# Performance work log

Hardware: AMD Instinct MI355X
Metric: run time of the kernel (lower is better)

Reference implementation:

```python
import jax, jax.numpy as jnp
import numpy as np

D = 256          # d_embed
KD = 256         # key_d_embed
NHEAD = 8
DK = D // NHEAD  # 32
QH = QW = 128
QWS = 16
KH = KW = 64
KWS = 8
R = QWS // KWS   # qk_ratio = 2
SCALE = 1.0 / np.sqrt(DK)


def _rel_index():
    # query coords on fine grid, key coords scaled up by ratio R
    qc = np.stack(np.meshgrid(np.arange(QWS), np.arange(QWS), indexing='ij'), -1).reshape(-1, 2)
    kc = np.stack(np.meshgrid(np.arange(KWS), np.arange(KWS), indexing='ij'), -1).reshape(-1, 2) * R
    rel = qc[:, None, :] - kc[None, :, :] + (QWS - R)  # values in [0, 2*QWS-R-1]
    return jnp.asarray(rel[..., 0] * (2 * QWS - R) + rel[..., 1])  # (QWS^2, KWS^2)


def _partition(t, ws):
    # (B, h, H, W, d) -> (B, h, H/ws, W/ws, ws*ws, d)
    B, h, H, W, d = t.shape
    t = t.reshape(B, h, H // ws, ws, W // ws, ws, d).transpose(0, 1, 2, 4, 3, 5, 6)
    return t.reshape(B, h, H // ws, W // ws, ws * ws, d)


def _merge(t, ws, H, W):
    # inverse of _partition
    B, h, nH, nW, _, d = t.shape
    t = t.reshape(B, h, nH, nW, ws, ws, d).transpose(0, 1, 2, 4, 3, 5, 6)
    return t.reshape(B, h, H, W, d)


def setup_inputs() -> dict:
    key = jax.random.key(0)
    ks = jax.random.split(key, 9)
    x = jax.random.normal(ks[0], (8, QH, QW, D), dtype=jnp.float32)
    z = jax.random.normal(ks[1], (8, KH, KW, KD), dtype=jnp.float32)
    mask = jax.random.randint(ks[2], (1, NHEAD, QH // QWS, QW // QWS, QWS * QWS, KWS * KWS), 0, 2) == 1
    Wq = jax.random.normal(ks[3], (D, D), dtype=jnp.float32) * 0.02
    bq = jnp.zeros((D,), dtype=jnp.float32)
    Wkv = jax.random.normal(ks[4], (KD, 2 * D), dtype=jnp.float32) * 0.02
    bkv = jnp.zeros((2 * D,), dtype=jnp.float32)
    Wo = jax.random.normal(ks[5], (D, D), dtype=jnp.float32) * 0.02
    bo = jnp.zeros((D,), dtype=jnp.float32)
    rel_table = jax.random.normal(ks[6], ((2 * QWS - R) ** 2, NHEAD), dtype=jnp.float32) * 0.02
    return {"x": x, "z": z, "mask": mask, "Wq": Wq, "bq": bq, "Wkv": Wkv, "bkv": bkv, "Wo": Wo, "bo": bo, "rel_table": rel_table}


def reference(x, z, mask, Wq, bq, Wkv, bkv, Wo, bo, rel_table):
    B, H, W, _ = x.shape
    q = (x @ Wq + bq).reshape(B, H, W, NHEAD, DK).transpose(0, 3, 1, 2, 4)        # (B,h,H,W,dk)
    kv = (z @ Wkv + bkv).reshape(B, KH, KW, 2, NHEAD, DK).transpose(3, 0, 4, 1, 2, 5)
    k, v = kv[0], kv[1]                                                           # (B,h,_H,_W,dk)
    sq, sk = QWS // 2, KWS // 2
    q = jnp.roll(q, (-sq, -sq), axis=(2, 3))
    k = jnp.roll(k, (-sk, -sk), axis=(2, 3))
    v = jnp.roll(v, (-sk, -sk), axis=(2, 3))
    q = _partition(q, QWS)   # (B,h,nh,nw,QWS^2,dk)
    k = _partition(k, KWS)   # (B,h,nh,nw,KWS^2,dk)
    v = _partition(v, KWS)
    attn = jnp.einsum('bhnmqd,bhnmkd->bhnmqk', q, k) * SCALE
    bias = rel_table[_rel_index()].transpose(2, 0, 1)[None, :, None, None]        # (1,h,1,1,QWS^2,KWS^2)
    attn = attn + bias
    attn = jnp.where(mask, jnp.float32(-1e9), attn)
    attn = jax.nn.softmax(attn, axis=-1)
    out = jnp.einsum('bhnmqk,bhnmkd->bhnmqd', attn, v)
    out = _merge(out, QWS, H, W)
    out = jnp.roll(out, (sq, sq), axis=(2, 3))
    out = out.transpose(0, 2, 3, 1, 4).reshape(B, H, W, D)
    return out @ Wo + bo
```

## Files before the change

kernel.cpp:

```cpp
#include <hip/hip_runtime.h>
#include <hip/hip_bf16.h>
#include <type_traits>


typedef __attribute__((ext_vector_type(8))) short short8v;
typedef __attribute__((ext_vector_type(4))) float f32x4;
typedef __attribute__((ext_vector_type(8))) unsigned short ushort8v;
typedef __attribute__((ext_vector_type(4))) unsigned short ushort4v;

#define DEV __device__ __forceinline__

DEV unsigned short f2bf(float f) {
    union { float f; unsigned u; } v; v.f = f;
    unsigned r = v.u + 0x7FFFu + ((v.u >> 16) & 1u);
    return (unsigned short)(r >> 16);
}

__global__ void prep_weights(const float* __restrict__ Wq, const float* __restrict__ Wkv,
                             const float* __restrict__ Wo,
                             unsigned short* __restrict__ WqT, unsigned short* __restrict__ WkvT,
                             unsigned short* __restrict__ WoT) {
    int idx = blockIdx.x * 256 + threadIdx.x;
    if (idx < 65536) {
        int n = idx >> 8, k = idx & 255;
        WqT[idx] = f2bf(Wq[k * 256 + n]);
    } else if (idx < 196608) {
        int i = idx - 65536;
        int n = i >> 8, k = i & 255;
        WkvT[i] = f2bf(Wkv[k * 512 + n]);
    } else {
        int i = idx - 196608;
        int n = i >> 8, k = i & 255;
        WoT[i] = f2bf(Wo[k * 256 + n]);
    }
}

__global__ void prep_bias(const float* __restrict__ rel_table, float* __restrict__ biasb) {
    int idx = blockIdx.x * 256 + threadIdx.x;
    int head = idx >> 14;
    int q = (idx >> 6) & 255;
    int k = idx & 63;
    int qi = q >> 4, qj = q & 15;
    int ki = k >> 3, kj = k & 7;
    int r0 = qi - 2 * ki + 14, r1 = qj - 2 * kj + 14;
    biasb[idx] = rel_table[(r0 * 30 + r1) * 8 + head];
}

template <typename InT, bool OUT_BF16>
__global__ __launch_bounds__(256) void gemm_proj(
    const InT* __restrict__ A, const unsigned short* __restrict__ BT,
    const float* __restrict__ bias, void* __restrict__ Cout,
    int M, int N, int K)
{
    __shared__ __align__(16) unsigned short As[128][40];
    __shared__ __align__(16) unsigned short Bs[128][40];

    const int tid = threadIdx.x;
    const int mb = blockIdx.y * 128;
    const int nb = blockIdx.x * 128;
    const int w = tid >> 6, lane = tid & 63, lr = lane & 15, lg = lane >> 4;
    const int wm = (w >> 1) * 64, wn = (w & 1) * 64;

    f32x4 acc[4][4];
#pragma unroll
    for (int i = 0; i < 4; ++i)
#pragma unroll
        for (int j = 0; j < 4; ++j) acc[i][j] = {0.f, 0.f, 0.f, 0.f};

    for (int kb = 0; kb < K; kb += 32) {
        if constexpr (std::is_same<InT, float>::value) {
#pragma unroll
            for (int i = 0; i < 4; ++i) {
                int row = (tid >> 3) + i * 32;
                int c4 = (tid & 7) * 4;
                const float4 v = *reinterpret_cast<const float4*>(
                    &A[(size_t)(mb + row) * K + kb + c4]);
                ushort4v u = { f2bf(v.x), f2bf(v.y), f2bf(v.z), f2bf(v.w) };
                *reinterpret_cast<ushort4v*>(&As[row][c4]) = u;
            }
        } else {
#pragma unroll
            for (int i = 0; i < 2; ++i) {
                int flat = tid + i * 256;
                int row = flat >> 2, c8 = (flat & 3) * 8;
                ushort8v v = *reinterpret_cast<const ushort8v*>(
                    &A[(size_t)(mb + row) * K + kb + c8]);
                *reinterpret_cast<ushort8v*>(&As[row][c8]) = v;
            }
        }
#pragma unroll
        for (int i = 0; i < 2; ++i) {
            int flat = tid + i * 256;
            int row = flat >> 2, c8 = (flat & 3) * 8;
            ushort8v v = *reinterpret_cast<const ushort8v*>(
                &BT[(size_t)(nb + row) * K + kb + c8]);
            *reinterpret_cast<ushort8v*>(&Bs[row][c8]) = v;
        }
        __syncthreads();

        short8v af[4], bfr[4];
#pragma unroll
        for (int mt = 0; mt < 4; ++mt)
            af[mt] = *reinterpret_cast<const short8v*>(&As[wm + mt * 16 + lr][lg * 8]);
#pragma unroll
        for (int nt = 0; nt < 4; ++nt)
            bfr[nt] = *reinterpret_cast<const short8v*>(&Bs[wn + nt * 16 + lr][lg * 8]);
#pragma unroll
        for (int mt = 0; mt < 4; ++mt)
#pragma unroll
            for (int nt = 0; nt < 4; ++nt)
                acc[mt][nt] = __builtin_amdgcn_mfma_f32_16x16x32_bf16(
                    af[mt], bfr[nt], acc[mt][nt], 0, 0, 0);
        __syncthreads();
    }

#pragma unroll
    for (int mt = 0; mt < 4; ++mt)
#pragma unroll
        for (int nt = 0; nt < 4; ++nt)
#pragma unroll
            for (int j = 0; j < 4; ++j) {
                int row = mb + wm + mt * 16 + lg * 4 + j;
                int col = nb + wn + nt * 16 + lr;
                float v = acc[mt][nt][j] + bias[col];
                if constexpr (OUT_BF16)
                    ((unsigned short*)Cout)[(size_t)row * N + col] = f2bf(v);
                else
                    ((float*)Cout)[(size_t)row * N + col] = v;
            }
}

__global__ __launch_bounds__(256) void win_attn(
    unsigned short* __restrict__ Qbuf,
    const unsigned short* __restrict__ KVbuf,
    const int* __restrict__ mask,
    const float* __restrict__ biasb)
{
    __shared__ __align__(16) unsigned char sQP[256 * 144];
    __shared__ __align__(16) unsigned short Ks[64][40];
    __shared__ __align__(16) unsigned short Vt[32][72];
    auto Qs = reinterpret_cast<unsigned short(*)[40]>(sQP);
    auto Ps = reinterpret_cast<unsigned short(*)[72]>(sQP);

    const int tid = threadIdx.x;
    const int win = blockIdx.x, head = blockIdx.y, b = blockIdx.z;
    const int wi = win >> 3, wj = win & 7;

    {
        int li = tid >> 4, lj = tid & 15;
        int gr = (wi * 16 + li + 8) & 127;
        int gc = (wj * 16 + lj + 8) & 127;
        const unsigned short* src =
            Qbuf + ((size_t)(b * 16384 + gr * 128 + gc)) * 256 + head * 32;
#pragma unroll
        for (int c = 0; c < 4; ++c)
            *reinterpret_cast<ushort8v*>(&Qs[tid][c * 8]) =
                *reinterpret_cast<const ushort8v*>(src + c * 8);
    }
    if (tid < 64) {
        int ki = tid >> 3, kj = tid & 7;
        int kr = (wi * 8 + ki + 4) & 63;
        int kc = (wj * 8 + kj + 4) & 63;
        const unsigned short* src =
            KVbuf + ((size_t)(b * 4096 + kr * 64 + kc)) * 512 + head * 32;
#pragma unroll
        for (int c = 0; c < 4; ++c)
            *reinterpret_cast<ushort8v*>(&Ks[tid][c * 8]) =
                *reinterpret_cast<const ushort8v*>(src + c * 8);
    } else if (tid < 128) {
        int key = tid - 64;
        int ki = key >> 3, kj = key & 7;
        int kr = (wi * 8 + ki + 4) & 63;
        int kc = (wj * 8 + kj + 4) & 63;
        const unsigned short* src =
            KVbuf + ((size_t)(b * 4096 + kr * 64 + kc)) * 512 + 256 + head * 32;
#pragma unroll
        for (int c = 0; c < 4; ++c) {
            ushort8v v = *reinterpret_cast<const ushort8v*>(src + c * 8);
#pragma unroll
            for (int e = 0; e < 8; ++e) Vt[c * 8 + e][key] = v[e];
        }
    }
    __syncthreads();

    const int w = tid >> 6, lane = tid & 63, lr = lane & 15, lg = lane >> 4;
    const int qb = w * 64;

    short8v qf[4], kf[4];
#pragma unroll
    for (int mt = 0; mt < 4; ++mt)
        qf[mt] = *reinterpret_cast<const short8v*>(&Qs[qb + mt * 16 + lr][lg * 8]);
#pragma unroll
    for (int nt = 0; nt < 4; ++nt)
        kf[nt] = *reinterpret_cast<const short8v*>(&Ks[nt * 16 + lr][lg * 8]);

    f32x4 s[4][4];
#pragma unroll
    for (int mt = 0; mt < 4; ++mt)
#pragma unroll
        for (int nt = 0; nt < 4; ++nt) s[mt][nt] = {0.f, 0.f, 0.f, 0.f};
#pragma unroll
    for (int mt = 0; mt < 4; ++mt)
#pragma unroll
        for (int nt = 0; nt < 4; ++nt)
            s[mt][nt] = __builtin_amdgcn_mfma_f32_16x16x32_bf16(qf[mt], kf[nt], s[mt][nt], 0, 0, 0);

    __syncthreads();

    const float scale = 0.17677669529663687f;
#pragma unroll
    for (int mt = 0; mt < 4; ++mt) {
#pragma unroll
        for (int j = 0; j < 4; ++j) {
            int q = qb + mt * 16 + lg * 4 + j;
            float v[4];
            float m = -3.0e38f;
#pragma unroll
            for (int nt = 0; nt < 4; ++nt) {
                int key = nt * 16 + lr;
                float bi = biasb[(head * 256 + q) * 64 + key];
                int mk = mask[(((head * 64 + win) * 256 + q) * 64) + key];
                float sv = s[mt][nt][j] * scale + bi;
                if (mk) sv = -1.0e9f;
                v[nt] = sv;
                m = fmaxf(m, sv);
            }
#pragma unroll
            for (int d = 1; d < 16; d <<= 1) m = fmaxf(m, __shfl_xor(m, d, 64));
            float sum = 0.f;
#pragma unroll
            for (int nt = 0; nt < 4; ++nt) { v[nt] = __expf(v[nt] - m); sum += v[nt]; }
#pragma unroll
            for (int d = 1; d < 16; d <<= 1) sum += __shfl_xor(sum, d, 64);
            float inv = 1.0f / sum;
#pragma unroll
            for (int nt = 0; nt < 4; ++nt)
                Ps[q][nt * 16 + lr] = f2bf(v[nt] * inv);
        }
    }

    f32x4 o[4][2];
#pragma unroll
    for (int mt = 0; mt < 4; ++mt)
#pragma unroll
        for (int nt = 0; nt < 2; ++nt) o[mt][nt] = {0.f, 0.f, 0.f, 0.f};
#pragma unroll
    for (int kc = 0; kc < 2; ++kc) {
        short8v pf[4], vf[2];
#pragma unroll
        for (int mt = 0; mt < 4; ++mt)
            pf[mt] = *reinterpret_cast<const short8v*>(&Ps[qb + mt * 16 + lr][kc * 32 + lg * 8]);
#pragma unroll
        for (int nt = 0; nt < 2; ++nt)
            vf[nt] = *reinterpret_cast<const short8v*>(&Vt[nt * 16 + lr][kc * 32 + lg * 8]);
#pragma unroll
        for (int mt = 0; mt < 4; ++mt)
#pragma unroll
            for (int nt = 0; nt < 2; ++nt)
                o[mt][nt] = __builtin_amdgcn_mfma_f32_16x16x32_bf16(pf[mt], vf[nt], o[mt][nt], 0, 0, 0);
    }

#pragma unroll
    for (int mt = 0; mt < 4; ++mt)
#pragma unroll
        for (int nt = 0; nt < 2; ++nt)
#pragma unroll
            for (int j = 0; j < 4; ++j) {
                int q = qb + mt * 16 + lg * 4 + j;
                int li = q >> 4, lj = q & 15;
                int gr = (wi * 16 + li + 8) & 127;
                int gc = (wj * 16 + lj + 8) & 127;
                int dk = nt * 16 + lr;
                Qbuf[((size_t)(b * 16384 + gr * 128 + gc)) * 256 + head * 32 + dk] =
                    f2bf(o[mt][nt][j]);
            }
}

extern "C" void kernel_launch(void* const* d_in, const int* in_sizes, int n_in,
                              void* d_out, int out_size, void* d_ws, size_t ws_size,
                              hipStream_t stream) {
    const float* x    = (const float*)d_in[0];
    const float* z    = (const float*)d_in[1];
    const int*   mask = (const int*)d_in[2];
    const float* Wq   = (const float*)d_in[3];
    const float* bq   = (const float*)d_in[4];
    const float* Wkv  = (const float*)d_in[5];
    const float* bkv  = (const float*)d_in[6];
    const float* Wo   = (const float*)d_in[7];
    const float* bo   = (const float*)d_in[8];
    const float* rel  = (const float*)d_in[9];
    float* out = (float*)d_out;

    char* ws = (char*)d_ws;
    unsigned short* Qbuf  = (unsigned short*)(ws);
    unsigned short* KVbuf = (unsigned short*)(ws + 67108864);
    unsigned short* WqT   = (unsigned short*)(ws + 100663296);
    unsigned short* WkvT  = (unsigned short*)(ws + 100794368);
    unsigned short* WoT   = (unsigned short*)(ws + 101056512);
    float*          biasb = (float*)(ws + 101187584);

    prep_weights<<<1024, 256, 0, stream>>>(Wq, Wkv, Wo, WqT, WkvT, WoT);
    prep_bias<<<512, 256, 0, stream>>>(rel, biasb);

    gemm_proj<float, true><<<dim3(2, 1024), 256, 0, stream>>>(
        x, WqT, bq, (void*)Qbuf, 131072, 256, 256);
    gemm_proj<float, true><<<dim3(4, 256), 256, 0, stream>>>(
        z, WkvT, bkv, (void*)KVbuf, 32768, 512, 256);
    win_attn<<<dim3(64, 8, 8), 256, 0, stream>>>(Qbuf, KVbuf, mask, biasb);
    gemm_proj<unsigned short, false><<<dim3(2, 1024), 256, 0, stream>>>(
        Qbuf, WoT, bo, (void*)out, 131072, 256, 256);
}
```

Before: 226.2 us.

## Bit-pack mask, fold scale into Wq, load Q/K fragments directly from global

Packs the int32 attention mask into 64-bit bitmasks once per call, so each row costs one 8-byte load instead of 64 int loads. Folds the softmax scale into Wq and bq during weight prep, and loads the Q and K MFMA fragments straight from global memory instead of staging them in LDS, which removes one barrier. The P buffer gets an XOR swizzle to avoid bank conflicts, and s_setprio is raised around the MFMA blocks. The cost is an extra mask-packing kernel per call and uncoalesced direct global fragment loads.

```diff
diff --git a/kernel.cpp b/kernel.cpp
--- a/kernel.cpp
+++ b/kernel.cpp
@@ -15,6 +15,8 @@
     unsigned r = v.u + 0x7FFFu + ((v.u >> 16) & 1u);
     return (unsigned short)(r >> 16);
 }
+
+#define ATT_SCALE 0.17677669529663687f
 
 __global__ void prep_weights(const float* __restrict__ Wq, const float* __restrict__ Wkv,
                              const float* __restrict__ Wo,
@@ -23,7 +25,7 @@
     int idx = blockIdx.x * 256 + threadIdx.x;
     if (idx < 65536) {
         int n = idx >> 8, k = idx & 255;
-        WqT[idx] = f2bf(Wq[k * 256 + n]);
+        WqT[idx] = f2bf(Wq[k * 256 + n] * ATT_SCALE);
     } else if (idx < 196608) {
         int i = idx - 65536;
         int n = i >> 8, k = i & 255;
@@ -35,15 +37,36 @@
     }
 }
 
-__global__ void prep_bias(const float* __restrict__ rel_table, float* __restrict__ biasb) {
+__global__ void prep_bias(const float* __restrict__ rel_table, const float* __restrict__ bq,
+                          float* __restrict__ biasb, float* __restrict__ bqs) {
     int idx = blockIdx.x * 256 + threadIdx.x;
-    int head = idx >> 14;
-    int q = (idx >> 6) & 255;
-    int k = idx & 63;
-    int qi = q >> 4, qj = q & 15;
-    int ki = k >> 3, kj = k & 7;
-    int r0 = qi - 2 * ki + 14, r1 = qj - 2 * kj + 14;
-    biasb[idx] = rel_table[(r0 * 30 + r1) * 8 + head];
+    if (idx < 131072) {
+        int head = idx >> 14;
+        int q = (idx >> 6) & 255;
+        int k = idx & 63;
+        int qi = q >> 4, qj = q & 15;
+        int ki = k >> 3, kj = k & 7;
+        int r0 = qi - 2 * ki + 14, r1 = qj - 2 * kj + 14;
+        biasb[idx] = rel_table[(r0 * 30 + r1) * 8 + head];
+    } else if (idx < 131328) {
+        int i = idx - 131072;
+        bqs[i] = bq[i] * ATT_SCALE;
+    }
+}
+
+__global__ void prep_mask(const int* __restrict__ mask, unsigned long long* __restrict__ mp) {
+    int idx = blockIdx.x * 256 + threadIdx.x;
+    const int4* src = reinterpret_cast<const int4*>(mask + (size_t)idx * 64);
+    unsigned long long bits = 0;
+#pragma unroll
+    for (int c = 0; c < 16; ++c) {
+        int4 v = src[c];
+        if (v.x) bits |= 1ull << (c * 4 + 0);
+        if (v.y) bits |= 1ull << (c * 4 + 1);
+        if (v.z) bits |= 1ull << (c * 4 + 2);
+        if (v.w) bits |= 1ull << (c * 4 + 3);
+    }
+    mp[idx] = bits;
 }
 
 template <typename InT, bool OUT_BF16>
@@ -133,95 +156,74 @@
 __global__ __launch_bounds__(256) void win_attn(
     unsigned short* __restrict__ Qbuf,
     const unsigned short* __restrict__ KVbuf,
-    const int* __restrict__ mask,
+    const unsigned long long* __restrict__ maskp,
     const float* __restrict__ biasb)
 {
-    __shared__ __align__(16) unsigned char sQP[256 * 144];
-    __shared__ __align__(16) unsigned short Ks[64][40];
+    __shared__ __align__(16) unsigned char Pb[256 * 128];
     __shared__ __align__(16) unsigned short Vt[32][72];
-    auto Qs = reinterpret_cast<unsigned short(*)[40]>(sQP);
-    auto Ps = reinterpret_cast<unsigned short(*)[72]>(sQP);
 
     const int tid = threadIdx.x;
     const int win = blockIdx.x, head = blockIdx.y, b = blockIdx.z;
     const int wi = win >> 3, wj = win & 7;
-
-    {
-        int li = tid >> 4, lj = tid & 15;
-        int gr = (wi * 16 + li + 8) & 127;
-        int gc = (wj * 16 + lj + 8) & 127;
-        const unsigned short* src =
-            Qbuf + ((size_t)(b * 16384 + gr * 128 + gc)) * 256 + head * 32;
-#pragma unroll
-        for (int c = 0; c < 4; ++c)
-            *reinterpret_cast<ushort8v*>(&Qs[tid][c * 8]) =
-                *reinterpret_cast<const ushort8v*>(src + c * 8);
-    }
-    if (tid < 64) {
-        int ki = tid >> 3, kj = tid & 7;
-        int kr = (wi * 8 + ki + 4) & 63;
-        int kc = (wj * 8 + kj + 4) & 63;
-        const unsigned short* src =
-            KVbuf + ((size_t)(b * 4096 + kr * 64 + kc)) * 512 + head * 32;
-#pragma unroll
-        for (int c = 0; c < 4; ++c)
-            *reinterpret_cast<ushort8v*>(&Ks[tid][c * 8]) =
-                *reinterpret_cast<const ushort8v*>(src + c * 8);
-    } else if (tid < 128) {
-        int key = tid - 64;
-        int ki = key >> 3, kj = key & 7;
-        int kr = (wi * 8 + ki + 4) & 63;
-        int kc = (wj * 8 + kj + 4) & 63;
-        const unsigned short* src =
-            KVbuf + ((size_t)(b * 4096 + kr * 64 + kc)) * 512 + 256 + head * 32;
-#pragma unroll
-        for (int c = 0; c < 4; ++c) {
-            ushort8v v = *reinterpret_cast<const ushort8v*>(src + c * 8);
-#pragma unroll
-            for (int e = 0; e < 8; ++e) Vt[c * 8 + e][key] = v[e];
-        }
-    }
-    __syncthreads();
-
     const int w = tid >> 6, lane = tid & 63, lr = lane & 15, lg = lane >> 4;
     const int qb = w * 64;
 
+    {
+        int key = tid & 63, c = tid >> 6;
+        int kr = (wi * 8 + (key >> 3) + 4) & 63;
+        int kc = (wj * 8 + (key & 7) + 4) & 63;
+        ushort8v v = *reinterpret_cast<const ushort8v*>(
+            KVbuf + ((size_t)(b * 4096 + kr * 64 + kc)) * 512 + 256 + head * 32 + c * 8);
+#pragma unroll
+        for (int e = 0; e < 8; ++e) Vt[c * 8 + e][key] = v[e];
+    }
+
     short8v qf[4], kf[4];
 #pragma unroll
-    for (int mt = 0; mt < 4; ++mt)
-        qf[mt] = *reinterpret_cast<const short8v*>(&Qs[qb + mt * 16 + lr][lg * 8]);
-#pragma unroll
-    for (int nt = 0; nt < 4; ++nt)
-        kf[nt] = *reinterpret_cast<const short8v*>(&Ks[nt * 16 + lr][lg * 8]);
+    for (int mt = 0; mt < 4; ++mt) {
+        int q = qb + mt * 16 + lr;
+        int gr = (wi * 16 + (q >> 4) + 8) & 127;
+        int gc = (wj * 16 + (q & 15) + 8) & 127;
+        qf[mt] = *reinterpret_cast<const short8v*>(
+            Qbuf + ((size_t)(b * 16384 + gr * 128 + gc)) * 256 + head * 32 + lg * 8);
+    }
+#pragma unroll
+    for (int nt = 0; nt < 4; ++nt) {
+        int key = nt * 16 + lr;
+        int kr = (wi * 8 + (key >> 3) + 4) & 63;
+        int kc = (wj * 8 + (key & 7) + 4) & 63;
+        kf[nt] = *reinterpret_cast<const short8v*>(
+            KVbuf + ((size_t)(b * 4096 + kr * 64 + kc)) * 512 + head * 32 + lg * 8);
+    }
 
     f32x4 s[4][4];
 #pragma unroll
     for (int mt = 0; mt < 4; ++mt)
 #pragma unroll
         for (int nt = 0; nt < 4; ++nt) s[mt][nt] = {0.f, 0.f, 0.f, 0.f};
+    __builtin_amdgcn_s_setprio(1);
 #pragma unroll
     for (int mt = 0; mt < 4; ++mt)
 #pragma unroll
         for (int nt = 0; nt < 4; ++nt)
             s[mt][nt] = __builtin_amdgcn_mfma_f32_16x16x32_bf16(qf[mt], kf[nt], s[mt][nt], 0, 0, 0);
-
-    __syncthreads();
-
-    const float scale = 0.17677669529663687f;
+    __builtin_amdgcn_s_setprio(0);
+
+    const unsigned long long* mrow = maskp + (size_t)(head * 64 + win) * 256;
 #pragma unroll
     for (int mt = 0; mt < 4; ++mt) {
 #pragma unroll
         for (int j = 0; j < 4; ++j) {
             int q = qb + mt * 16 + lg * 4 + j;
+            unsigned long long mb = mrow[q];
+            const float* brow = biasb + (size_t)(head * 256 + q) * 64;
             float v[4];
             float m = -3.0e38f;
 #pragma unroll
             for (int nt = 0; nt < 4; ++nt) {
                 int key = nt * 16 + lr;
-                float bi = biasb[(head * 256 + q) * 64 + key];
-                int mk = mask[(((head * 64 + win) * 256 + q) * 64) + key];
-                float sv = s[mt][nt][j] * scale + bi;
-                if (mk) sv = -1.0e9f;
+                float sv = s[mt][nt][j] + brow[key];
+                if ((mb >> key) & 1ull) sv = -1.0e9f;
                 v[nt] = sv;
                 m = fmaxf(m, sv);
             }
@@ -233,11 +235,16 @@
 #pragma unroll
             for (int d = 1; d < 16; d <<= 1) sum += __shfl_xor(sum, d, 64);
             float inv = 1.0f / sum;
-#pragma unroll
-            for (int nt = 0; nt < 4; ++nt)
-                Ps[q][nt * 16 + lr] = f2bf(v[nt] * inv);
-        }
-    }
+            int sw = (q & 7) << 4;
+#pragma unroll
+            for (int nt = 0; nt < 4; ++nt) {
+                int off = q * 128 + (((nt * 16 + lr) * 2) ^ sw);
+                *reinterpret_cast<unsigned short*>(Pb + off) = f2bf(v[nt] * inv);
+            }
+        }
+    }
+
+    __syncthreads();
 
     f32x4 o[4][2];
 #pragma unroll
@@ -248,32 +255,36 @@
     for (int kc = 0; kc < 2; ++kc) {
         short8v pf[4], vf[2];
 #pragma unroll
-        for (int mt = 0; mt < 4; ++mt)
-            pf[mt] = *reinterpret_cast<const short8v*>(&Ps[qb + mt * 16 + lr][kc * 32 + lg * 8]);
+        for (int mt = 0; mt < 4; ++mt) {
+            int row = qb + mt * 16 + lr;
+            int coff = (kc * 64 + lg * 16) ^ ((row & 7) << 4);
+            pf[mt] = *reinterpret_cast<const short8v*>(Pb + row * 128 + coff);
+        }
 #pragma unroll
         for (int nt = 0; nt < 2; ++nt)
             vf[nt] = *reinterpret_cast<const short8v*>(&Vt[nt * 16 + lr][kc * 32 + lg * 8]);
+        __builtin_amdgcn_s_setprio(1);
 #pragma unroll
         for (int mt = 0; mt < 4; ++mt)
 #pragma unroll
             for (int nt = 0; nt < 2; ++nt)
                 o[mt][nt] = __builtin_amdgcn_mfma_f32_16x16x32_bf16(pf[mt], vf[nt], o[mt][nt], 0, 0, 0);
-    }
-
-#pragma unroll
-    for (int mt = 0; mt < 4; ++mt)
-#pragma unroll
-        for (int nt = 0; nt < 2; ++nt)
-#pragma unroll
-            for (int j = 0; j < 4; ++j) {
-                int q = qb + mt * 16 + lg * 4 + j;
-                int li = q >> 4, lj = q & 15;
-                int gr = (wi * 16 + li + 8) & 127;
-                int gc = (wj * 16 + lj + 8) & 127;
-                int dk = nt * 16 + lr;
-                Qbuf[((size_t)(b * 16384 + gr * 128 + gc)) * 256 + head * 32 + dk] =
-                    f2bf(o[mt][nt][j]);
-            }
+        __builtin_amdgcn_s_setprio(0);
+    }
+
+#pragma unroll
+    for (int mt = 0; mt < 4; ++mt)
+#pragma unroll
+        for (int j = 0; j < 4; ++j) {
+            int q = qb + mt * 16 + lg * 4 + j;
+            int gr = (wi * 16 + (q >> 4) + 8) & 127;
+            int gc = (wj * 16 + (q & 15) + 8) & 127;
+            unsigned short* dst =
+                Qbuf + ((size_t)(b * 16384 + gr * 128 + gc)) * 256 + head * 32;
+#pragma unroll
+            for (int nt = 0; nt < 2; ++nt)
+                dst[nt * 16 + lr] = f2bf(o[mt][nt][j]);
+        }
 }
 
 extern "C" void kernel_launch(void* const* d_in, const int* in_sizes, int n_in,
@@ -292,21 +303,24 @@
     float* out = (float*)d_out;
 
     char* ws = (char*)d_ws;
-    unsigned short* Qbuf  = (unsigned short*)(ws);
-    unsigned short* KVbuf = (unsigned short*)(ws + 67108864);
-    unsigned short* WqT   = (unsigned short*)(ws + 100663296);
-    unsigned short* WkvT  = (unsigned short*)(ws + 100794368);
-    unsigned short* WoT   = (unsigned short*)(ws + 101056512);
-    float*          biasb = (float*)(ws + 101187584);
+    unsigned short*     Qbuf  = (unsigned short*)(ws);
+    unsigned short*     KVbuf = (unsigned short*)(ws + 67108864);
+    unsigned short*     WqT   = (unsigned short*)(ws + 100663296);
+    unsigned short*     WkvT  = (unsigned short*)(ws + 100794368);
+    unsigned short*     WoT   = (unsigned short*)(ws + 101056512);
+    float*              biasb = (float*)(ws + 101187584);
+    unsigned long long* maskp = (unsigned long long*)(ws + 101711872);
+    float*              bqs   = (float*)(ws + 102760448);
 
     prep_weights<<<1024, 256, 0, stream>>>(Wq, Wkv, Wo, WqT, WkvT, WoT);
-    prep_bias<<<512, 256, 0, stream>>>(rel, biasb);
+    prep_bias<<<513, 256, 0, stream>>>(rel, bq, biasb, bqs);
+    prep_mask<<<512, 256, 0, stream>>>(mask, maskp);
 
     gemm_proj<float, true><<<dim3(2, 1024), 256, 0, stream>>>(
-        x, WqT, bq, (void*)Qbuf, 131072, 256, 256);
+        x, WqT, bqs, (void*)Qbuf, 131072, 256, 256);
     gemm_proj<float, true><<<dim3(4, 256), 256, 0, stream>>>(
         z, WkvT, bkv, (void*)KVbuf, 32768, 512, 256);
-    win_attn<<<dim3(64, 8, 8), 256, 0, stream>>>(Qbuf, KVbuf, mask, biasb);
+    win_attn<<<dim3(64, 8, 8), 256, 0, stream>>>(Qbuf, KVbuf, maskp, biasb);
     gemm_proj<unsigned short, false><<<dim3(2, 1024), 256, 0, stream>>>(
         Qbuf, WoT, bo, (void*)out, 131072, 256, 256);
 }
```

New measurement: 222.1 us. About the same (-1.8%).
